# Kernel tuning notes

Hardware: AMD Instinct MI355X
Metric: run time of the kernel (lower is better)

## Reference

```python
import jax, jax.numpy as jnp
import numpy as np
from jax import lax

GAIN = 16.0           # encoder_gains[0]
TEMP = 0.3            # soft_round_temperature
MASK = 9              # mask_size
PAD = 4               # (MASK - 1) // 2
# dim_arm = 16 causal taps inside the 9x9 mask (all indices < center index 40)
CTX_IDX = [12, 13, 14, 20, 21, 22, 23, 24, 28, 29, 30, 31, 32, 33, 38, 39]
CTX_OFF = [(i // MASK, i % MASK) for i in CTX_IDX]
IMG_H, IMG_W = 1024, 1536
N_GRIDS = 7
SIZES = [(int(np.ceil(IMG_H / 2 ** i)), int(np.ceil(IMG_W / 2 ** i))) for i in range(N_GRIDS)]
N_TOTAL = sum(h * w for h, w in SIZES)  # 2097024


def _softround(x, t):
    fl = jnp.floor(x)
    return fl + 0.5 * jnp.tanh((x - fl - 0.5) / t) / jnp.tanh(0.5 / t) + 0.5


def _forward(latents, noise_u, arm_w1, arm_b1, arm_w2, arm_b2, arm_wo, arm_bo,
             ups_k, pre_k, syn_w1, syn_b1, syn_w2, syn_b2):
    # --- quantize latents: softround(softround(x*g) + kumaraswamy noise), a=1 -> uniform-0.5 ---
    flat = jnp.concatenate([l.reshape(-1) for l in latents]) * GAIN
    flat_q = _softround(_softround(flat, TEMP) + (noise_u - 0.5), TEMP)
    dec, cnt = [], 0
    for h, w in SIZES:
        dec.append(flat_q[cnt:cnt + h * w].reshape(1, 1, h, w))
        cnt += h * w
    # --- _get_neighbor: masked causal context gather (16 taps of the 9x9 mask) ---
    ctxs = []
    for l in dec:
        h, w = l.shape[2], l.shape[3]
        xp = jnp.pad(l[0, 0], PAD)  # zero pad, matches F.pad constant 0
        ctxs.append(jnp.stack([xp[dy:dy + h, dx:dx + w] for dy, dx in CTX_OFF], axis=-1).reshape(-1, len(CTX_OFF)))
    ctx = jnp.concatenate(ctxs, axis=0)  # [N, 16]
    # --- ARM MLP: residual hidden layers, final linear to (mu, log_scale) ---
    h1 = jax.nn.relu(ctx @ arm_w1.T + arm_b1 + ctx)
    h2 = jax.nn.relu(h1 @ arm_w2.T + arm_b2 + h1)
    raw = h2 @ arm_wo.T + arm_bo
    mu, log_s = raw[:, 0], raw[:, 1]
    scale = jnp.exp(-0.5 * jnp.clip(log_s, -13.8155, 13.8155))
    def lcdf(x):
        return 0.5 - 0.5 * jnp.sign(x - mu) * jnp.expm1(-jnp.abs(x - mu) / scale)
    proba = jnp.maximum(lcdf(flat_q + 0.5) - lcdf(flat_q - 0.5), 2.0 ** -16)
    rate = -jnp.log2(proba)
    # --- upsampling: coarse-to-fine, depthwise separable convT x2 + preconcat filter ---
    x = dec[-1]
    for step, i in enumerate(range(N_GRIDS - 1, 0, -1)):
        c = x.shape[1]
        kern = jnp.broadcast_to(jnp.outer(ups_k[step], ups_k[step])[None, None], (c, 1, 8, 8))
        x = lax.conv_general_dilated(x, kern, (1, 1), ((4, 4), (4, 4)), lhs_dilation=(2, 2),
                                     dimension_numbers=('NCHW', 'OIHW', 'NCHW'), feature_group_count=c)
        ht, wt = SIZES[i - 1]
        x = x[:, :, :ht, :wt]
        pk2 = jnp.outer(pre_k[step], pre_k[step])[None, None]  # (1,1,7,7)
        t = lax.conv_general_dilated(dec[i - 1], pk2, (1, 1), ((3, 3), (3, 3)),
                                     dimension_numbers=('NCHW', 'OIHW', 'NCHW'))
        x = jnp.concatenate([t, x], axis=1)
    # --- synthesis: 1x1 conv 7->48 relu, 48->6, split mean / log_scale ---
    hid = jax.nn.relu(jnp.einsum('bchw,oc->bohw', x, syn_w1) + syn_b1[None, :, None, None])
    out = jnp.einsum('bchw,oc->bohw', hid, syn_w2) + syn_b2[None, :, None, None]
    pixel_mean, pixel_log_scale = out[:, :3], out[:, 3:]
    # F.interpolate to img_size is identity here (already full resolution)
    decoded = jnp.clip(pixel_mean, 0.0, 1.0)
    return pixel_mean, pixel_log_scale, decoded, rate


def setup_inputs():
    key = jax.random.key(0)
    ks = jax.random.split(key, 16)
    d = {}
    for i, (h, w) in enumerate(SIZES):
        d['latent%d' % i] = jax.random.uniform(ks[i], (1, 1, h, w), jnp.float32, -0.5, 0.5)
    d['noise_u'] = jax.random.uniform(ks[7], (N_TOTAL,), jnp.float32)
    d['arm_w1'] = jax.random.normal(ks[8], (16, 16), jnp.float32) * 0.25
    d['arm_b1'] = jnp.zeros((16,), jnp.float32)
    d['arm_w2'] = jax.random.normal(ks[9], (16, 16), jnp.float32) * 0.25
    d['arm_b2'] = jnp.zeros((16,), jnp.float32)
    d['arm_wo'] = jax.random.normal(ks[10], (2, 16), jnp.float32) * 0.25
    d['arm_bo'] = jnp.zeros((2,), jnp.float32)
    d['ups_k'] = jax.random.normal(ks[11], (6, 8), jnp.float32) * 0.2 + 0.125
    d['pre_k'] = jax.random.normal(ks[12], (6, 7), jnp.float32) * 0.2 + 0.1
    d['syn_w1'] = jax.random.normal(ks[13], (48, 7), jnp.float32) * 0.3
    d['syn_b1'] = jnp.zeros((48,), jnp.float32)
    d['syn_w2'] = jax.random.normal(ks[14], (6, 48), jnp.float32) * 0.1
    d['syn_b2'] = jnp.zeros((6,), jnp.float32)
    return d


def reference(latent0, latent1, latent2, latent3, latent4, latent5, latent6, noise_u,
              arm_w1, arm_b1, arm_w2, arm_b2, arm_wo, arm_bo,
              ups_k, pre_k, syn_w1, syn_b1, syn_w2, syn_b2):
    return _forward([latent0, latent1, latent2, latent3, latent4, latent5, latent6], noise_u,
                    arm_w1, arm_b1, arm_w2, arm_b2, arm_wo, arm_bo,
                    ups_k, pre_k, syn_w1, syn_b1, syn_w2, syn_b2)
```

## Files before the change

kernel.cpp:

```cpp
#include <hip/hip_runtime.h>
#include <math.h>

#define N_TOTAL 2097024
#define HWF (1024 * 1536)

#define OFF0 0
#define OFF1 1572864
#define OFF2 1966080
#define OFF3 2064384
#define OFF4 2088960
#define OFF5 2095104
#define OFF6 2096640

#define OUT_LS   (3 * HWF)
#define OUT_DEC  (6 * HWF)
#define OUT_RATE (9 * HWF)

typedef float f4 __attribute__((ext_vector_type(4), aligned(4)));

__device__ __forceinline__ float softround_f(float x) {
    const float INV_T = 1.0f / 0.3f;
    const float HALF_OVER_TANH = 0.53699381f;
    float fl = floorf(x);
    return fl + tanhf((x - fl - 0.5f) * INV_T) * HALF_OVER_TANH + 0.5f;
}

__global__ void quant_kernel(const float* __restrict__ l0, const float* __restrict__ l1,
                             const float* __restrict__ l2, const float* __restrict__ l3,
                             const float* __restrict__ l4, const float* __restrict__ l5,
                             const float* __restrict__ l6, const float* __restrict__ noise,
                             float* __restrict__ flat_q) {
    int idx = blockIdx.x * blockDim.x + threadIdx.x;
    if (idx >= N_TOTAL) return;
    float v;
    if      (idx < OFF1) v = l0[idx - OFF0];
    else if (idx < OFF2) v = l1[idx - OFF1];
    else if (idx < OFF3) v = l2[idx - OFF2];
    else if (idx < OFF4) v = l3[idx - OFF3];
    else if (idx < OFF5) v = l4[idx - OFF4];
    else if (idx < OFF6) v = l5[idx - OFF5];
    else                 v = l6[idx - OFF6];
    float x = v * 16.0f;
    float s1 = softround_f(x);
    float s2 = softround_f(s1 + noise[idx] - 0.5f);
    flat_q[idx] = s2;
}

template <int H, int W, int OFFT>
__device__ __forceinline__ void arm_body(const float* __restrict__ flat_q, int pos,
                                         const float* __restrict__ w1, const float* __restrict__ b1,
                                         const float* __restrict__ w2, const float* __restrict__ b2,
                                         const float* __restrict__ wo, const float* __restrict__ bo,
                                         float* __restrict__ rate_out) {
    if (pos >= H * W) return;
    unsigned up = (unsigned)pos;
    int y = up / (unsigned)W;
    int x = pos - y * W;
    const float* g = flat_q + OFFT;

    const int DY[16] = {-3,-3,-3,-2,-2,-2,-2,-2,-1,-1,-1,-1,-1,-1, 0, 0};
    const int DX[16] = {-1, 0, 1,-2,-1, 0, 1, 2,-3,-2,-1, 0, 1, 2,-2,-1};
    float ctx[16];
#pragma unroll
    for (int k = 0; k < 16; k++) {
        int yy = y + DY[k], xx = x + DX[k];
        ctx[k] = (yy >= 0 && yy < H && xx >= 0 && xx < W) ? g[yy * W + xx] : 0.0f;
    }

    float h1[16];
#pragma unroll 4
    for (int j = 0; j < 16; j++) {
        float acc = b1[j] + ctx[j];
#pragma unroll
        for (int k = 0; k < 16; k++) acc = fmaf(w1[j * 16 + k], ctx[k], acc);
        h1[j] = fmaxf(acc, 0.0f);
    }
    float h2[16];
#pragma unroll 4
    for (int j = 0; j < 16; j++) {
        float acc = b2[j] + h1[j];
#pragma unroll
        for (int k = 0; k < 16; k++) acc = fmaf(w2[j * 16 + k], h1[k], acc);
        h2[j] = fmaxf(acc, 0.0f);
    }
    float mu = bo[0], ls = bo[1];
#pragma unroll
    for (int k = 0; k < 16; k++) {
        mu = fmaf(wo[k], h2[k], mu);
        ls = fmaf(wo[16 + k], h2[k], ls);
    }
    ls = fminf(fmaxf(ls, -13.8155f), 13.8155f);
    float inv_scale = expf(0.5f * ls);

    float q = g[(size_t)y * W + x];
    float da = (q + 0.5f) - mu;
    float db = (q - 0.5f) - mu;
    float la = 0.5f - 0.5f * copysignf(1.0f, da) * expm1f(-fabsf(da) * inv_scale);
    float lb = 0.5f - 0.5f * copysignf(1.0f, db) * expm1f(-fabsf(db) * inv_scale);
    float proba = fmaxf(la - lb, 1.52587890625e-05f);
    rate_out[OFFT + pos] = -log2f(proba);
}

__global__ __launch_bounds__(256) void arm_all_kernel(
    const float* __restrict__ flat_q,
    const float* __restrict__ w1, const float* __restrict__ b1,
    const float* __restrict__ w2, const float* __restrict__ b2,
    const float* __restrict__ wo, const float* __restrict__ bo,
    float* __restrict__ rate_out) {
    int b = blockIdx.x;
    int t = threadIdx.x;
    if (b < 6144) {
        arm_body<1024, 1536, OFF0>(flat_q, b * 256 + t, w1, b1, w2, b2, wo, bo, rate_out);
    } else if (b < 7680) {
        arm_body<512, 768, OFF1>(flat_q, (b - 6144) * 256 + t, w1, b1, w2, b2, wo, bo, rate_out);
    } else if (b < 8064) {
        arm_body<256, 384, OFF2>(flat_q, (b - 7680) * 256 + t, w1, b1, w2, b2, wo, bo, rate_out);
    } else if (b < 8160) {
        arm_body<128, 192, OFF3>(flat_q, (b - 8064) * 256 + t, w1, b1, w2, b2, wo, bo, rate_out);
    } else if (b < 8184) {
        arm_body<64, 96, OFF4>(flat_q, (b - 8160) * 256 + t, w1, b1, w2, b2, wo, bo, rate_out);
    } else if (b < 8190) {
        arm_body<32, 48, OFF5>(flat_q, (b - 8184) * 256 + t, w1, b1, w2, b2, wo, bo, rate_out);
    } else {
        arm_body<16, 24, OFF6>(flat_q, (b - 8190) * 256 + t, w1, b1, w2, b2, wo, bo, rate_out);
    }
}

__device__ __forceinline__ void up_quad(const float* __restrict__ in, int H, int W,
                                        int i, int j, const float* K, float o[4]) {
    float w[5][5];
    bool interior = (i >= 2 && i <= H - 3 && j >= 2 && j <= W - 3);
    if (interior) {
        const float* p = in + (i - 2) * W + (j - 2);
#pragma unroll
        for (int r = 0; r < 5; r++) {
            f4 a = *(const f4*)p;
            w[r][0] = a.x; w[r][1] = a.y; w[r][2] = a.z; w[r][3] = a.w;
            w[r][4] = p[4];
            p += W;
        }
    } else {
#pragma unroll
        for (int r = 0; r < 5; r++)
#pragma unroll
            for (int e = 0; e < 5; e++) {
                int yy = i - 2 + r, xx = j - 2 + e;
                w[r][e] = (yy >= 0 && yy < H && xx >= 0 && xx < W) ? in[yy * W + xx] : 0.0f;
            }
    }
    float h0[5], h1[5];
#pragma unroll
    for (int r = 0; r < 5; r++) {
        h0[r] = K[0]*w[r][0] + K[2]*w[r][1] + K[4]*w[r][2] + K[6]*w[r][3];
        h1[r] = K[1]*w[r][1] + K[3]*w[r][2] + K[5]*w[r][3] + K[7]*w[r][4];
    }
    o[0] = K[0]*h0[0] + K[2]*h0[1] + K[4]*h0[2] + K[6]*h0[3];
    o[1] = K[0]*h1[0] + K[2]*h1[1] + K[4]*h1[2] + K[6]*h1[3];
    o[2] = K[1]*h0[1] + K[3]*h0[2] + K[5]*h0[3] + K[7]*h0[4];
    o[3] = K[1]*h1[1] + K[3]*h1[2] + K[5]*h1[3] + K[7]*h1[4];
}

__device__ __forceinline__ void conv7_quad(const float* __restrict__ dec, int H, int W,
                                           int i, int j, const float* k, float o[4]) {
    int Y = 2 * i, X = 2 * j;
    float g0[8], g1[8];
    bool interior = (Y - 3 >= 0 && Y + 4 <= H - 1 && X - 3 >= 0 && X + 4 <= W - 1);
    if (interior) {
        const float* p = dec + (Y - 3) * W + (X - 3);
#pragma unroll
        for (int r = 0; r < 8; r++) {
            f4 a = *(const f4*)p;
            f4 b = *(const f4*)(p + 4);
            g0[r] = k[0]*a.x + k[1]*a.y + k[2]*a.z + k[3]*a.w + k[4]*b.x + k[5]*b.y + k[6]*b.z;
            g1[r] = k[0]*a.y + k[1]*a.z + k[2]*a.w + k[3]*b.x + k[4]*b.y + k[5]*b.z + k[6]*b.w;
            p += W;
        }
    } else {
#pragma unroll
        for (int r = 0; r < 8; r++) {
            float wv[8];
#pragma unroll
            for (int q = 0; q < 8; q++) {
                int yy = Y - 3 + r, xx = X - 3 + q;
                wv[q] = (yy >= 0 && yy < H && xx >= 0 && xx < W) ? dec[yy * W + xx] : 0.0f;
            }
            g0[r] = k[0]*wv[0] + k[1]*wv[1] + k[2]*wv[2] + k[3]*wv[3] + k[4]*wv[4] + k[5]*wv[5] + k[6]*wv[6];
            g1[r] = k[0]*wv[1] + k[1]*wv[2] + k[2]*wv[3] + k[3]*wv[4] + k[4]*wv[5] + k[5]*wv[6] + k[6]*wv[7];
        }
    }
    o[0] = k[0]*g0[0] + k[1]*g0[1] + k[2]*g0[2] + k[3]*g0[3] + k[4]*g0[4] + k[5]*g0[5] + k[6]*g0[6];
    o[1] = k[0]*g1[0] + k[1]*g1[1] + k[2]*g1[2] + k[3]*g1[3] + k[4]*g1[4] + k[5]*g1[5] + k[6]*g1[6];
    o[2] = k[0]*g0[1] + k[1]*g0[2] + k[2]*g0[3] + k[3]*g0[4] + k[4]*g0[5] + k[5]*g0[6] + k[6]*g0[7];
    o[3] = k[0]*g1[1] + k[1]*g1[2] + k[2]*g1[3] + k[3]*g1[4] + k[4]*g1[5] + k[5]*g1[6] + k[6]*g1[7];
}

__global__ void pyramid_quad_kernel(const float* __restrict__ xin, int hin, int win_,
                                    const float* __restrict__ dec,
                                    const float* __restrict__ upsk, const float* __restrict__ prek,
                                    float* __restrict__ xout, int hout, int wout) {
    int qw = wout >> 1, qh = hout >> 1;
    int j = blockIdx.x * blockDim.x + threadIdx.x;
    int i = blockIdx.y * blockDim.y + threadIdx.y;
    int c = blockIdx.z;
    if (j >= qw || i >= qh) return;
    float o[4];
    if (c == 0) {
        float k[7];
#pragma unroll
        for (int p = 0; p < 7; p++) k[p] = prek[p];
        conv7_quad(dec, hout, wout, i, j, k, o);
    } else {
        float K[8];
#pragma unroll
        for (int p = 0; p < 8; p++) K[p] = upsk[p];
        up_quad(xin + (size_t)(c - 1) * hin * win_, hin, win_, i, j, K, o);
    }
    size_t base = ((size_t)c * hout + 2 * i) * wout + 2 * j;
    *(float2*)(xout + base)        = make_float2(o[0], o[1]);
    *(float2*)(xout + base + wout) = make_float2(o[2], o[3]);
}

__global__ __launch_bounds__(256) void final_kernel(
    const float* __restrict__ up_in,
    const float* __restrict__ dec0,
    const float* __restrict__ upsk, const float* __restrict__ prek,
    const float* __restrict__ w1, const float* __restrict__ b1,
    const float* __restrict__ w2, const float* __restrict__ b2,
    float* __restrict__ out) {
    const int H2_ = 512, W2_ = 768, H1_ = 1024, W1_ = 1536;
    int t = threadIdx.x;
    int j = blockIdx.x * 16 + (t & 15);
    int i = blockIdx.y * 16 + (t >> 4);

    float K[8], kp[7];
#pragma unroll
    for (int p = 0; p < 8; p++) K[p] = upsk[p];
#pragma unroll
    for (int p = 0; p < 7; p++) kp[p] = prek[p];

    float px0[7], px1[7], px2[7], px3[7];
    {
        float o[4];
        conv7_quad(dec0, H1_, W1_, i, j, kp, o);
        px0[0] = o[0]; px1[0] = o[1]; px2[0] = o[2]; px3[0] = o[3];
    }
#pragma unroll
    for (int c = 0; c < 6; c++) {
        float o[4];
        up_quad(up_in + (size_t)c * (H2_ * W2_), H2_, W2_, i, j, K, o);
        px0[c + 1] = o[0]; px1[c + 1] = o[1]; px2[c + 1] = o[2]; px3[c + 1] = o[3];
    }

    float o0[6], o1[6], o2[6], o3[6];
#pragma unroll
    for (int q = 0; q < 6; q++) {
        float bq = b2[q];
        o0[q] = bq; o1[q] = bq; o2[q] = bq; o3[q] = bq;
    }
#pragma unroll 4
    for (int k = 0; k < 48; k++) {
        float bk = b1[k];
        float a0 = bk, a1 = bk, a2 = bk, a3 = bk;
#pragma unroll
        for (int c = 0; c < 7; c++) {
            float wk = w1[k * 7 + c];
            a0 = fmaf(wk, px0[c], a0);
            a1 = fmaf(wk, px1[c], a1);
            a2 = fmaf(wk, px2[c], a2);
            a3 = fmaf(wk, px3[c], a3);
        }
        a0 = fmaxf(a0, 0.0f); a1 = fmaxf(a1, 0.0f); a2 = fmaxf(a2, 0.0f); a3 = fmaxf(a3, 0.0f);
#pragma unroll
        for (int q = 0; q < 6; q++) {
            float wj = w2[q * 48 + k];
            o0[q] = fmaf(wj, a0, o0[q]);
            o1[q] = fmaf(wj, a1, o1[q]);
            o2[q] = fmaf(wj, a2, o2[q]);
            o3[q] = fmaf(wj, a3, o3[q]);
        }
    }

    size_t base = (size_t)(2 * i) * W1_ + 2 * j;
#pragma unroll
    for (int c = 0; c < 3; c++) {
        *(float2*)(out + (size_t)c * HWF + base)       = make_float2(o0[c], o1[c]);
        *(float2*)(out + (size_t)c * HWF + base + W1_) = make_float2(o2[c], o3[c]);
        *(float2*)(out + OUT_LS + (size_t)c * HWF + base)       = make_float2(o0[c + 3], o1[c + 3]);
        *(float2*)(out + OUT_LS + (size_t)c * HWF + base + W1_) = make_float2(o2[c + 3], o3[c + 3]);
        *(float2*)(out + OUT_DEC + (size_t)c * HWF + base) =
            make_float2(fminf(fmaxf(o0[c], 0.0f), 1.0f), fminf(fmaxf(o1[c], 0.0f), 1.0f));
        *(float2*)(out + OUT_DEC + (size_t)c * HWF + base + W1_) =
            make_float2(fminf(fmaxf(o2[c], 0.0f), 1.0f), fminf(fmaxf(o3[c], 0.0f), 1.0f));
    }
}

extern "C" void kernel_launch(void* const* d_in, const int* in_sizes, int n_in,
                              void* d_out, int out_size, void* d_ws, size_t ws_size,
                              hipStream_t stream) {
    const float* lat[7];
    for (int i = 0; i < 7; i++) lat[i] = (const float*)d_in[i];
    const float* noise  = (const float*)d_in[7];
    const float* arm_w1 = (const float*)d_in[8];
    const float* arm_b1 = (const float*)d_in[9];
    const float* arm_w2 = (const float*)d_in[10];
    const float* arm_b2 = (const float*)d_in[11];
    const float* arm_wo = (const float*)d_in[12];
    const float* arm_bo = (const float*)d_in[13];
    const float* ups_k  = (const float*)d_in[14];
    const float* pre_k  = (const float*)d_in[15];
    const float* syn_w1 = (const float*)d_in[16];
    const float* syn_b1 = (const float*)d_in[17];
    const float* syn_w2 = (const float*)d_in[18];
    const float* syn_b2 = (const float*)d_in[19];
    float* out = (float*)d_out;

    float* flat_q = (float*)d_ws;
    float* bufA   = flat_q + N_TOTAL;
    float* bufB   = bufA + 6 * 512 * 768;

    static const int SH[7]  = {1024, 512, 256, 128, 64, 32, 16};
    static const int SW[7]  = {1536, 768, 384, 192, 96, 48, 24};
    static const int OFF[7] = {OFF0, OFF1, OFF2, OFF3, OFF4, OFF5, OFF6};

    quant_kernel<<<(N_TOTAL + 255) / 256, 256, 0, stream>>>(
        lat[0], lat[1], lat[2], lat[3], lat[4], lat[5], lat[6], noise, flat_q);

    arm_all_kernel<<<8192, 256, 0, stream>>>(flat_q, arm_w1, arm_b1, arm_w2, arm_b2,
                                             arm_wo, arm_bo, out + OUT_RATE);

    const float* xin = flat_q + OFF6;
    float* bufs[2] = {bufA, bufB};
    for (int s = 0; s < 5; s++) {
        int i    = 6 - s;
        int hin  = SH[i], win_ = SW[i];
        int hout = SH[i - 1], wout = SW[i - 1];
        int cin  = s + 1;
        float* xout = bufs[s & 1];
        dim3 blk(16, 16);
        dim3 grd((wout / 2 + 15) / 16, (hout / 2 + 15) / 16, cin + 1);
        pyramid_quad_kernel<<<grd, blk, 0, stream>>>(xin, hin, win_,
                                                     flat_q + OFF[i - 1],
                                                     ups_k + s * 8, pre_k + s * 7,
                                                     xout, hout, wout);
        xin = xout;
    }

    dim3 fgrd(768 / 16, 512 / 16);
    final_kernel<<<fgrd, 256, 0, stream>>>(bufA, flat_q,
                                           ups_k + 5 * 8, pre_k + 5 * 7,
                                           syn_w1, syn_b1, syn_w2, syn_b2, out);
}
```

Before: 149.6 us.

## Use packed FP32 math across ARM, upsampling and synthesis kernels

Rewrites the ARM MLP so each thread handles two adjacent pixels using 2-wide float vectors, which are meant to map to packed FP32 FMA instructions. It adds an interior fast path that loads the context taps as vectors, and halves the ARM grid to match. The upsampling, conv7 and synthesis MLP inner loops are also reorganised around packed FMAs. Softround replaces tanhf with an exp/reciprocal formulation, which may slightly change numerical accuracy; processing two pixels per thread also raises register pressure.

```diff
diff --git a/kernel.cpp b/kernel.cpp
--- a/kernel.cpp
+++ b/kernel.cpp
@@ -16,13 +16,22 @@
 #define OUT_DEC  (6 * HWF)
 #define OUT_RATE (9 * HWF)
 
-typedef float f4 __attribute__((ext_vector_type(4), aligned(4)));
+typedef float f4  __attribute__((ext_vector_type(4), aligned(4)));
+typedef float pf2 __attribute__((ext_vector_type(2), aligned(4)));
+
+__device__ __forceinline__ pf2 splat2(float s) { return (pf2){s, s}; }
+__device__ __forceinline__ pf2 pk_fma(pf2 a, pf2 b, pf2 c) { return __builtin_elementwise_fma(a, b, c); }
+__device__ __forceinline__ pf2 pk_max(pf2 a, pf2 b) { return __builtin_elementwise_max(a, b); }
+__device__ __forceinline__ pf2 pk_min(pf2 a, pf2 b) { return __builtin_elementwise_min(a, b); }
 
 __device__ __forceinline__ float softround_f(float x) {
     const float INV_T = 1.0f / 0.3f;
     const float HALF_OVER_TANH = 0.53699381f;
     float fl = floorf(x);
-    return fl + tanhf((x - fl - 0.5f) * INV_T) * HALF_OVER_TANH + 0.5f;
+    float z = (x - fl - 0.5f) * INV_T;
+    float e = __expf(2.0f * z);
+    float th = 1.0f - 2.0f * __builtin_amdgcn_rcpf(e + 1.0f);
+    return fl + th * HALF_OVER_TANH + 0.5f;
 }
 
 __global__ void quant_kernel(const float* __restrict__ l0, const float* __restrict__ l1,
@@ -47,58 +56,77 @@
 }
 
 template <int H, int W, int OFFT>
-__device__ __forceinline__ void arm_body(const float* __restrict__ flat_q, int pos,
-                                         const float* __restrict__ w1, const float* __restrict__ b1,
-                                         const float* __restrict__ w2, const float* __restrict__ b2,
-                                         const float* __restrict__ wo, const float* __restrict__ bo,
-                                         float* __restrict__ rate_out) {
-    if (pos >= H * W) return;
-    unsigned up = (unsigned)pos;
-    int y = up / (unsigned)W;
+__device__ __forceinline__ void arm_body2(const float* __restrict__ flat_q, int pair,
+                                          const float* __restrict__ w1, const float* __restrict__ b1,
+                                          const float* __restrict__ w2, const float* __restrict__ b2,
+                                          const float* __restrict__ wo, const float* __restrict__ bo,
+                                          float* __restrict__ rate_out) {
+    constexpr int NPAIR = H * W / 2;
+    if (pair >= NPAIR) return;
+    int pos = 2 * pair;
+    int y = (unsigned)pos / (unsigned)W;
     int x = pos - y * W;
     const float* g = flat_q + OFFT;
 
     const int DY[16] = {-3,-3,-3,-2,-2,-2,-2,-2,-1,-1,-1,-1,-1,-1, 0, 0};
     const int DX[16] = {-1, 0, 1,-2,-1, 0, 1, 2,-3,-2,-1, 0, 1, 2,-2,-1};
-    float ctx[16];
-#pragma unroll
-    for (int k = 0; k < 16; k++) {
-        int yy = y + DY[k], xx = x + DX[k];
-        ctx[k] = (yy >= 0 && yy < H && xx >= 0 && xx < W) ? g[yy * W + xx] : 0.0f;
-    }
-
-    float h1[16];
+    pf2 ctx[16];
+    bool interior = (y >= 3) && (x >= 3) && (x <= W - 4);
+    if (interior) {
+#pragma unroll
+        for (int k = 0; k < 16; k++)
+            ctx[k] = *(const pf2*)&g[(y + DY[k]) * W + x + DX[k]];
+    } else {
+#pragma unroll
+        for (int k = 0; k < 16; k++) {
+            int yy = y + DY[k];
+            float lo = 0.0f, hi = 0.0f;
+            if (yy >= 0) {
+                int xx = x + DX[k];
+                if (xx >= 0 && xx < W)          lo = g[yy * W + xx];
+                if (xx + 1 >= 0 && xx + 1 < W)  hi = g[yy * W + xx + 1];
+            }
+            ctx[k] = (pf2){lo, hi};
+        }
+    }
+
+    pf2 h1[16];
 #pragma unroll 4
     for (int j = 0; j < 16; j++) {
-        float acc = b1[j] + ctx[j];
-#pragma unroll
-        for (int k = 0; k < 16; k++) acc = fmaf(w1[j * 16 + k], ctx[k], acc);
-        h1[j] = fmaxf(acc, 0.0f);
-    }
-    float h2[16];
+        pf2 acc = splat2(b1[j]) + ctx[j];
+#pragma unroll
+        for (int k = 0; k < 16; k++) acc = pk_fma(splat2(w1[j * 16 + k]), ctx[k], acc);
+        h1[j] = pk_max(acc, splat2(0.0f));
+    }
+    pf2 h2[16];
 #pragma unroll 4
     for (int j = 0; j < 16; j++) {
-        float acc = b2[j] + h1[j];
-#pragma unroll
-        for (int k = 0; k < 16; k++) acc = fmaf(w2[j * 16 + k], h1[k], acc);
-        h2[j] = fmaxf(acc, 0.0f);
-    }
-    float mu = bo[0], ls = bo[1];
+        pf2 acc = splat2(b2[j]) + h1[j];
+#pragma unroll
+        for (int k = 0; k < 16; k++) acc = pk_fma(splat2(w2[j * 16 + k]), h1[k], acc);
+        h2[j] = pk_max(acc, splat2(0.0f));
+    }
+    pf2 mu = splat2(bo[0]), ls = splat2(bo[1]);
 #pragma unroll
     for (int k = 0; k < 16; k++) {
-        mu = fmaf(wo[k], h2[k], mu);
-        ls = fmaf(wo[16 + k], h2[k], ls);
-    }
-    ls = fminf(fmaxf(ls, -13.8155f), 13.8155f);
-    float inv_scale = expf(0.5f * ls);
-
-    float q = g[(size_t)y * W + x];
-    float da = (q + 0.5f) - mu;
-    float db = (q - 0.5f) - mu;
-    float la = 0.5f - 0.5f * copysignf(1.0f, da) * expm1f(-fabsf(da) * inv_scale);
-    float lb = 0.5f - 0.5f * copysignf(1.0f, db) * expm1f(-fabsf(db) * inv_scale);
-    float proba = fmaxf(la - lb, 1.52587890625e-05f);
-    rate_out[OFFT + pos] = -log2f(proba);
+        mu = pk_fma(splat2(wo[k]), h2[k], mu);
+        ls = pk_fma(splat2(wo[16 + k]), h2[k], ls);
+    }
+
+    pf2 q = *(const pf2*)&g[pos];
+    pf2 rate;
+#pragma unroll
+    for (int c = 0; c < 2; c++) {
+        float lsc = fminf(fmaxf(ls[c], -13.8155f), 13.8155f);
+        float inv_scale = __expf(0.5f * lsc);
+        float da = (q[c] + 0.5f) - mu[c];
+        float db = (q[c] - 0.5f) - mu[c];
+        float la = 0.5f - 0.5f * copysignf(1.0f, da) * expm1f(-fabsf(da) * inv_scale);
+        float lb = 0.5f - 0.5f * copysignf(1.0f, db) * expm1f(-fabsf(db) * inv_scale);
+        float proba = fmaxf(la - lb, 1.52587890625e-05f);
+        rate[c] = -log2f(proba);
+    }
+    *(pf2*)&rate_out[OFFT + pos] = rate;
 }
 
 __global__ __launch_bounds__(256) void arm_all_kernel(
@@ -109,25 +137,25 @@
     float* __restrict__ rate_out) {
     int b = blockIdx.x;
     int t = threadIdx.x;
-    if (b < 6144) {
-        arm_body<1024, 1536, OFF0>(flat_q, b * 256 + t, w1, b1, w2, b2, wo, bo, rate_out);
-    } else if (b < 7680) {
-        arm_body<512, 768, OFF1>(flat_q, (b - 6144) * 256 + t, w1, b1, w2, b2, wo, bo, rate_out);
-    } else if (b < 8064) {
-        arm_body<256, 384, OFF2>(flat_q, (b - 7680) * 256 + t, w1, b1, w2, b2, wo, bo, rate_out);
-    } else if (b < 8160) {
-        arm_body<128, 192, OFF3>(flat_q, (b - 8064) * 256 + t, w1, b1, w2, b2, wo, bo, rate_out);
-    } else if (b < 8184) {
-        arm_body<64, 96, OFF4>(flat_q, (b - 8160) * 256 + t, w1, b1, w2, b2, wo, bo, rate_out);
-    } else if (b < 8190) {
-        arm_body<32, 48, OFF5>(flat_q, (b - 8184) * 256 + t, w1, b1, w2, b2, wo, bo, rate_out);
+    if (b < 3072) {
+        arm_body2<1024, 1536, OFF0>(flat_q, b * 256 + t, w1, b1, w2, b2, wo, bo, rate_out);
+    } else if (b < 3840) {
+        arm_body2<512, 768, OFF1>(flat_q, (b - 3072) * 256 + t, w1, b1, w2, b2, wo, bo, rate_out);
+    } else if (b < 4032) {
+        arm_body2<256, 384, OFF2>(flat_q, (b - 3840) * 256 + t, w1, b1, w2, b2, wo, bo, rate_out);
+    } else if (b < 4080) {
+        arm_body2<128, 192, OFF3>(flat_q, (b - 4032) * 256 + t, w1, b1, w2, b2, wo, bo, rate_out);
+    } else if (b < 4092) {
+        arm_body2<64, 96, OFF4>(flat_q, (b - 4080) * 256 + t, w1, b1, w2, b2, wo, bo, rate_out);
+    } else if (b < 4095) {
+        arm_body2<32, 48, OFF5>(flat_q, (b - 4092) * 256 + t, w1, b1, w2, b2, wo, bo, rate_out);
     } else {
-        arm_body<16, 24, OFF6>(flat_q, (b - 8190) * 256 + t, w1, b1, w2, b2, wo, bo, rate_out);
-    }
-}
-
-__device__ __forceinline__ void up_quad(const float* __restrict__ in, int H, int W,
-                                        int i, int j, const float* K, float o[4]) {
+        arm_body2<16, 24, OFF6>(flat_q, (b - 4095) * 256 + t, w1, b1, w2, b2, wo, bo, rate_out);
+    }
+}
+
+__device__ __forceinline__ void up_quad_pk(const float* __restrict__ in, int H, int W,
+                                           int i, int j, const float* K, pf2& o01, pf2& o23) {
     float w[5][5];
     bool interior = (i >= 2 && i <= H - 3 && j >= 2 && j <= W - 3);
     if (interior) {
@@ -148,50 +176,56 @@
                 w[r][e] = (yy >= 0 && yy < H && xx >= 0 && xx < W) ? in[yy * W + xx] : 0.0f;
             }
     }
-    float h0[5], h1[5];
+    pf2 h01[5];
 #pragma unroll
     for (int r = 0; r < 5; r++) {
-        h0[r] = K[0]*w[r][0] + K[2]*w[r][1] + K[4]*w[r][2] + K[6]*w[r][3];
-        h1[r] = K[1]*w[r][1] + K[3]*w[r][2] + K[5]*w[r][3] + K[7]*w[r][4];
-    }
-    o[0] = K[0]*h0[0] + K[2]*h0[1] + K[4]*h0[2] + K[6]*h0[3];
-    o[1] = K[0]*h1[0] + K[2]*h1[1] + K[4]*h1[2] + K[6]*h1[3];
-    o[2] = K[1]*h0[1] + K[3]*h0[2] + K[5]*h0[3] + K[7]*h0[4];
-    o[3] = K[1]*h1[1] + K[3]*h1[2] + K[5]*h1[3] + K[7]*h1[4];
-}
-
-__device__ __forceinline__ void conv7_quad(const float* __restrict__ dec, int H, int W,
-                                           int i, int j, const float* k, float o[4]) {
+        pf2 acc = splat2(0.0f);
+#pragma unroll
+        for (int e = 0; e < 4; e++)
+            acc = pk_fma((pf2){K[2 * e], K[2 * e + 1]}, (pf2){w[r][e], w[r][e + 1]}, acc);
+        h01[r] = acc;
+    }
+    o01 = splat2(0.0f); o23 = splat2(0.0f);
+#pragma unroll
+    for (int d = 0; d < 4; d++) {
+        o01 = pk_fma(splat2(K[2 * d]),     h01[d],     o01);
+        o23 = pk_fma(splat2(K[2 * d + 1]), h01[d + 1], o23);
+    }
+}
+
+__device__ __forceinline__ void conv7_quad_pk(const float* __restrict__ dec, int H, int W,
+                                              int i, int j, const float* k, pf2& o01, pf2& o23) {
     int Y = 2 * i, X = 2 * j;
-    float g0[8], g1[8];
+    pf2 g01[8];
     bool interior = (Y - 3 >= 0 && Y + 4 <= H - 1 && X - 3 >= 0 && X + 4 <= W - 1);
-    if (interior) {
-        const float* p = dec + (Y - 3) * W + (X - 3);
-#pragma unroll
-        for (int r = 0; r < 8; r++) {
+#pragma unroll
+    for (int r = 0; r < 8; r++) {
+        float wv[8];
+        if (interior) {
+            const float* p = dec + (Y - 3 + r) * W + (X - 3);
             f4 a = *(const f4*)p;
             f4 b = *(const f4*)(p + 4);
-            g0[r] = k[0]*a.x + k[1]*a.y + k[2]*a.z + k[3]*a.w + k[4]*b.x + k[5]*b.y + k[6]*b.z;
-            g1[r] = k[0]*a.y + k[1]*a.z + k[2]*a.w + k[3]*b.x + k[4]*b.y + k[5]*b.z + k[6]*b.w;
-            p += W;
-        }
-    } else {
-#pragma unroll
-        for (int r = 0; r < 8; r++) {
-            float wv[8];
+            wv[0] = a.x; wv[1] = a.y; wv[2] = a.z; wv[3] = a.w;
+            wv[4] = b.x; wv[5] = b.y; wv[6] = b.z; wv[7] = b.w;
+        } else {
 #pragma unroll
             for (int q = 0; q < 8; q++) {
                 int yy = Y - 3 + r, xx = X - 3 + q;
                 wv[q] = (yy >= 0 && yy < H && xx >= 0 && xx < W) ? dec[yy * W + xx] : 0.0f;
             }
-            g0[r] = k[0]*wv[0] + k[1]*wv[1] + k[2]*wv[2] + k[3]*wv[3] + k[4]*wv[4] + k[5]*wv[5] + k[6]*wv[6];
-            g1[r] = k[0]*wv[1] + k[1]*wv[2] + k[2]*wv[3] + k[3]*wv[4] + k[4]*wv[5] + k[5]*wv[6] + k[6]*wv[7];
-        }
-    }
-    o[0] = k[0]*g0[0] + k[1]*g0[1] + k[2]*g0[2] + k[3]*g0[3] + k[4]*g0[4] + k[5]*g0[5] + k[6]*g0[6];
-    o[1] = k[0]*g1[0] + k[1]*g1[1] + k[2]*g1[2] + k[3]*g1[3] + k[4]*g1[4] + k[5]*g1[5] + k[6]*g1[6];
-    o[2] = k[0]*g0[1] + k[1]*g0[2] + k[2]*g0[3] + k[3]*g0[4] + k[4]*g0[5] + k[5]*g0[6] + k[6]*g0[7];
-    o[3] = k[0]*g1[1] + k[1]*g1[2] + k[2]*g1[3] + k[3]*g1[4] + k[4]*g1[5] + k[5]*g1[6] + k[6]*g1[7];
+        }
+        pf2 acc = splat2(0.0f);
+#pragma unroll
+        for (int q = 0; q < 7; q++)
+            acc = pk_fma(splat2(k[q]), (pf2){wv[q], wv[q + 1]}, acc);
+        g01[r] = acc;
+    }
+    o01 = splat2(0.0f); o23 = splat2(0.0f);
+#pragma unroll
+    for (int r = 0; r < 7; r++) {
+        o01 = pk_fma(splat2(k[r]), g01[r],     o01);
+        o23 = pk_fma(splat2(k[r]), g01[r + 1], o23);
+    }
 }
 
 __global__ void pyramid_quad_kernel(const float* __restrict__ xin, int hin, int win_,
@@ -203,21 +237,21 @@
     int i = blockIdx.y * blockDim.y + threadIdx.y;
     int c = blockIdx.z;
     if (j >= qw || i >= qh) return;
-    float o[4];
+    pf2 o01, o23;
     if (c == 0) {
         float k[7];
 #pragma unroll
         for (int p = 0; p < 7; p++) k[p] = prek[p];
-        conv7_quad(dec, hout, wout, i, j, k, o);
+        conv7_quad_pk(dec, hout, wout, i, j, k, o01, o23);
     } else {
         float K[8];
 #pragma unroll
         for (int p = 0; p < 8; p++) K[p] = upsk[p];
-        up_quad(xin + (size_t)(c - 1) * hin * win_, hin, win_, i, j, K, o);
+        up_quad_pk(xin + (size_t)(c - 1) * hin * win_, hin, win_, i, j, K, o01, o23);
     }
     size_t base = ((size_t)c * hout + 2 * i) * wout + 2 * j;
-    *(float2*)(xout + base)        = make_float2(o[0], o[1]);
-    *(float2*)(xout + base + wout) = make_float2(o[2], o[3]);
+    *(pf2*)(xout + base)        = o01;
+    *(pf2*)(xout + base + wout) = o23;
 }
 
 __global__ __launch_bounds__(256) void final_kernel(
@@ -238,59 +272,45 @@
 #pragma unroll
     for (int p = 0; p < 7; p++) kp[p] = prek[p];
 
-    float px0[7], px1[7], px2[7], px3[7];
-    {
-        float o[4];
-        conv7_quad(dec0, H1_, W1_, i, j, kp, o);
-        px0[0] = o[0]; px1[0] = o[1]; px2[0] = o[2]; px3[0] = o[3];
-    }
-#pragma unroll
-    for (int c = 0; c < 6; c++) {
-        float o[4];
-        up_quad(up_in + (size_t)c * (H2_ * W2_), H2_, W2_, i, j, K, o);
-        px0[c + 1] = o[0]; px1[c + 1] = o[1]; px2[c + 1] = o[2]; px3[c + 1] = o[3];
-    }
-
-    float o0[6], o1[6], o2[6], o3[6];
-#pragma unroll
-    for (int q = 0; q < 6; q++) {
-        float bq = b2[q];
-        o0[q] = bq; o1[q] = bq; o2[q] = bq; o3[q] = bq;
-    }
+    pf2 px01[7], px23[7];
+    conv7_quad_pk(dec0, H1_, W1_, i, j, kp, px01[0], px23[0]);
+#pragma unroll
+    for (int c = 0; c < 6; c++)
+        up_quad_pk(up_in + (size_t)c * (H2_ * W2_), H2_, W2_, i, j, K, px01[c + 1], px23[c + 1]);
+
+    pf2 o01[6], o23[6];
+#pragma unroll
+    for (int q = 0; q < 6; q++) { o01[q] = splat2(b2[q]); o23[q] = splat2(b2[q]); }
 #pragma unroll 4
     for (int k = 0; k < 48; k++) {
-        float bk = b1[k];
-        float a0 = bk, a1 = bk, a2 = bk, a3 = bk;
+        pf2 a01 = splat2(b1[k]), a23 = a01;
 #pragma unroll
         for (int c = 0; c < 7; c++) {
-            float wk = w1[k * 7 + c];
-            a0 = fmaf(wk, px0[c], a0);
-            a1 = fmaf(wk, px1[c], a1);
-            a2 = fmaf(wk, px2[c], a2);
-            a3 = fmaf(wk, px3[c], a3);
-        }
-        a0 = fmaxf(a0, 0.0f); a1 = fmaxf(a1, 0.0f); a2 = fmaxf(a2, 0.0f); a3 = fmaxf(a3, 0.0f);
+            pf2 wk = splat2(w1[k * 7 + c]);
+            a01 = pk_fma(wk, px01[c], a01);
+            a23 = pk_fma(wk, px23[c], a23);
+        }
+        a01 = pk_max(a01, splat2(0.0f));
+        a23 = pk_max(a23, splat2(0.0f));
 #pragma unroll
         for (int q = 0; q < 6; q++) {
-            float wj = w2[q * 48 + k];
-            o0[q] = fmaf(wj, a0, o0[q]);
-            o1[q] = fmaf(wj, a1, o1[q]);
-            o2[q] = fmaf(wj, a2, o2[q]);
-            o3[q] = fmaf(wj, a3, o3[q]);
+            pf2 wj = splat2(w2[q * 48 + k]);
+            o01[q] = pk_fma(wj, a01, o01[q]);
+            o23[q] = pk_fma(wj, a23, o23[q]);
         }
     }
 
     size_t base = (size_t)(2 * i) * W1_ + 2 * j;
 #pragma unroll
     for (int c = 0; c < 3; c++) {
-        *(float2*)(out + (size_t)c * HWF + base)       = make_float2(o0[c], o1[c]);
-        *(float2*)(out + (size_t)c * HWF + base + W1_) = make_float2(o2[c], o3[c]);
-        *(float2*)(out + OUT_LS + (size_t)c * HWF + base)       = make_float2(o0[c + 3], o1[c + 3]);
-        *(float2*)(out + OUT_LS + (size_t)c * HWF + base + W1_) = make_float2(o2[c + 3], o3[c + 3]);
-        *(float2*)(out + OUT_DEC + (size_t)c * HWF + base) =
-            make_float2(fminf(fmaxf(o0[c], 0.0f), 1.0f), fminf(fmaxf(o1[c], 0.0f), 1.0f));
-        *(float2*)(out + OUT_DEC + (size_t)c * HWF + base + W1_) =
-            make_float2(fminf(fmaxf(o2[c], 0.0f), 1.0f), fminf(fmaxf(o3[c], 0.0f), 1.0f));
+        *(pf2*)(out + (size_t)c * HWF + base)       = o01[c];
+        *(pf2*)(out + (size_t)c * HWF + base + W1_) = o23[c];
+        *(pf2*)(out + OUT_LS + (size_t)c * HWF + base)       = o01[c + 3];
+        *(pf2*)(out + OUT_LS + (size_t)c * HWF + base + W1_) = o23[c + 3];
+        *(pf2*)(out + OUT_DEC + (size_t)c * HWF + base) =
+            pk_min(pk_max(o01[c], splat2(0.0f)), splat2(1.0f));
+        *(pf2*)(out + OUT_DEC + (size_t)c * HWF + base + W1_) =
+            pk_min(pk_max(o23[c], splat2(0.0f)), splat2(1.0f));
     }
 }
 
@@ -325,7 +345,7 @@
     quant_kernel<<<(N_TOTAL + 255) / 256, 256, 0, stream>>>(
         lat[0], lat[1], lat[2], lat[3], lat[4], lat[5], lat[6], noise, flat_q);
 
-    arm_all_kernel<<<8192, 256, 0, stream>>>(flat_q, arm_w1, arm_b1, arm_w2, arm_b2,
+    arm_all_kernel<<<4096, 256, 0, stream>>>(flat_q, arm_w1, arm_b1, arm_w2, arm_b2,
                                              arm_wo, arm_bo, out + OUT_RATE);
 
     const float* xin = flat_q + OFF6;
```

Result: slower. 174.6 us (+16.8%).

## Merge ARM rate kernel into final synthesis kernel and use fast tanh

Applied to the files above, without the earlier changes.

Removes the standalone ARM kernel and appends its blocks to the final synthesis kernel, so one launch covers both and the heavy final blocks run alongside the ARM blocks. Softround's tanhf is replaced with an exp plus hardware reciprocal formulation to cut transcendental cost in the quantize kernel. The inv_scale line computes a fast exp that is immediately overwritten by the original expf, so that part does nothing. The fused kernel's register use is the larger of the two bodies, which may reduce occupancy for the ARM part, and the fast tanh slightly changes numerics.

```diff
diff --git a/kernel.cpp b/kernel.cpp
--- a/kernel.cpp
+++ b/kernel.cpp
@@ -22,7 +22,10 @@
     const float INV_T = 1.0f / 0.3f;
     const float HALF_OVER_TANH = 0.53699381f;
     float fl = floorf(x);
-    return fl + tanhf((x - fl - 0.5f) * INV_T) * HALF_OVER_TANH + 0.5f;
+    float z = (x - fl - 0.5f) * INV_T;
+    float e = __expf(2.0f * z);
+    float th = 1.0f - 2.0f * __builtin_amdgcn_rcpf(e + 1.0f);
+    return fl + th * HALF_OVER_TANH + 0.5f;
 }
 
 __global__ void quant_kernel(const float* __restrict__ l0, const float* __restrict__ l1,
@@ -90,7 +93,8 @@
         ls = fmaf(wo[16 + k], h2[k], ls);
     }
     ls = fminf(fmaxf(ls, -13.8155f), 13.8155f);
-    float inv_scale = expf(0.5f * ls);
+    float inv_scale = __expf(0.5f * ls * 1.44269504f * 0.69314718f);
+    inv_scale = expf(0.5f * ls);
 
     float q = g[(size_t)y * W + x];
     float da = (q + 0.5f) - mu;
@@ -99,31 +103,6 @@
     float lb = 0.5f - 0.5f * copysignf(1.0f, db) * expm1f(-fabsf(db) * inv_scale);
     float proba = fmaxf(la - lb, 1.52587890625e-05f);
     rate_out[OFFT + pos] = -log2f(proba);
-}
-
-__global__ __launch_bounds__(256) void arm_all_kernel(
-    const float* __restrict__ flat_q,
-    const float* __restrict__ w1, const float* __restrict__ b1,
-    const float* __restrict__ w2, const float* __restrict__ b2,
-    const float* __restrict__ wo, const float* __restrict__ bo,
-    float* __restrict__ rate_out) {
-    int b = blockIdx.x;
-    int t = threadIdx.x;
-    if (b < 6144) {
-        arm_body<1024, 1536, OFF0>(flat_q, b * 256 + t, w1, b1, w2, b2, wo, bo, rate_out);
-    } else if (b < 7680) {
-        arm_body<512, 768, OFF1>(flat_q, (b - 6144) * 256 + t, w1, b1, w2, b2, wo, bo, rate_out);
-    } else if (b < 8064) {
-        arm_body<256, 384, OFF2>(flat_q, (b - 7680) * 256 + t, w1, b1, w2, b2, wo, bo, rate_out);
-    } else if (b < 8160) {
-        arm_body<128, 192, OFF3>(flat_q, (b - 8064) * 256 + t, w1, b1, w2, b2, wo, bo, rate_out);
-    } else if (b < 8184) {
-        arm_body<64, 96, OFF4>(flat_q, (b - 8160) * 256 + t, w1, b1, w2, b2, wo, bo, rate_out);
-    } else if (b < 8190) {
-        arm_body<32, 48, OFF5>(flat_q, (b - 8184) * 256 + t, w1, b1, w2, b2, wo, bo, rate_out);
-    } else {
-        arm_body<16, 24, OFF6>(flat_q, (b - 8190) * 256 + t, w1, b1, w2, b2, wo, bo, rate_out);
-    }
 }
 
 __device__ __forceinline__ void up_quad(const float* __restrict__ in, int H, int W,
@@ -220,7 +199,7 @@
     *(float2*)(xout + base + wout) = make_float2(o[2], o[3]);
 }
 
-__global__ __launch_bounds__(256) void final_kernel(
+__device__ __forceinline__ void final_body(int b, int t,
     const float* __restrict__ up_in,
     const float* __restrict__ dec0,
     const float* __restrict__ upsk, const float* __restrict__ prek,
@@ -228,9 +207,11 @@
     const float* __restrict__ w2, const float* __restrict__ b2,
     float* __restrict__ out) {
     const int H2_ = 512, W2_ = 768, H1_ = 1024, W1_ = 1536;
-    int t = threadIdx.x;
-    int j = blockIdx.x * 16 + (t & 15);
-    int i = blockIdx.y * 16 + (t >> 4);
+    unsigned ub = (unsigned)b;
+    int by = ub / 48u;
+    int bx = b - by * 48;
+    int j = bx * 16 + (t & 15);
+    int i = by * 16 + (t >> 4);
 
     float K[8], kp[7];
 #pragma unroll
@@ -291,6 +272,40 @@
             make_float2(fminf(fmaxf(o0[c], 0.0f), 1.0f), fminf(fmaxf(o1[c], 0.0f), 1.0f));
         *(float2*)(out + OUT_DEC + (size_t)c * HWF + base + W1_) =
             make_float2(fminf(fmaxf(o2[c], 0.0f), 1.0f), fminf(fmaxf(o3[c], 0.0f), 1.0f));
+    }
+}
+
+__global__ __launch_bounds__(256) void mega_kernel(
+    const float* __restrict__ up_in, const float* __restrict__ flat_q,
+    const float* __restrict__ upsk, const float* __restrict__ prek,
+    const float* __restrict__ sw1, const float* __restrict__ sb1,
+    const float* __restrict__ sw2, const float* __restrict__ sb2,
+    const float* __restrict__ aw1, const float* __restrict__ ab1,
+    const float* __restrict__ aw2, const float* __restrict__ ab2,
+    const float* __restrict__ awo, const float* __restrict__ abo,
+    float* __restrict__ out) {
+    int b = blockIdx.x;
+    int t = threadIdx.x;
+    if (b < 1536) {
+        final_body(b, t, up_in, flat_q, upsk, prek, sw1, sb1, sw2, sb2, out);
+        return;
+    }
+    int ab = b - 1536;
+    float* rate_out = out + OUT_RATE;
+    if (ab < 6144) {
+        arm_body<1024, 1536, OFF0>(flat_q, ab * 256 + t, aw1, ab1, aw2, ab2, awo, abo, rate_out);
+    } else if (ab < 7680) {
+        arm_body<512, 768, OFF1>(flat_q, (ab - 6144) * 256 + t, aw1, ab1, aw2, ab2, awo, abo, rate_out);
+    } else if (ab < 8064) {
+        arm_body<256, 384, OFF2>(flat_q, (ab - 7680) * 256 + t, aw1, ab1, aw2, ab2, awo, abo, rate_out);
+    } else if (ab < 8160) {
+        arm_body<128, 192, OFF3>(flat_q, (ab - 8064) * 256 + t, aw1, ab1, aw2, ab2, awo, abo, rate_out);
+    } else if (ab < 8184) {
+        arm_body<64, 96, OFF4>(flat_q, (ab - 8160) * 256 + t, aw1, ab1, aw2, ab2, awo, abo, rate_out);
+    } else if (ab < 8190) {
+        arm_body<32, 48, OFF5>(flat_q, (ab - 8184) * 256 + t, aw1, ab1, aw2, ab2, awo, abo, rate_out);
+    } else {
+        arm_body<16, 24, OFF6>(flat_q, (ab - 8190) * 256 + t, aw1, ab1, aw2, ab2, awo, abo, rate_out);
     }
 }
 
@@ -325,9 +340,6 @@
     quant_kernel<<<(N_TOTAL + 255) / 256, 256, 0, stream>>>(
         lat[0], lat[1], lat[2], lat[3], lat[4], lat[5], lat[6], noise, flat_q);
 
-    arm_all_kernel<<<8192, 256, 0, stream>>>(flat_q, arm_w1, arm_b1, arm_w2, arm_b2,
-                                             arm_wo, arm_bo, out + OUT_RATE);
-
     const float* xin = flat_q + OFF6;
     float* bufs[2] = {bufA, bufB};
     for (int s = 0; s < 5; s++) {
@@ -345,8 +357,9 @@
         xin = xout;
     }
 
-    dim3 fgrd(768 / 16, 512 / 16);
-    final_kernel<<<fgrd, 256, 0, stream>>>(bufA, flat_q,
-                                           ups_k + 5 * 8, pre_k + 5 * 7,
-                                           syn_w1, syn_b1, syn_w2, syn_b2, out);
-}
+    mega_kernel<<<9728, 256, 0, stream>>>(bufA, flat_q,
+                                          ups_k + 5 * 8, pre_k + 5 * 7,
+                                          syn_w1, syn_b1, syn_w2, syn_b2,
+                                          arm_w1, arm_b1, arm_w2, arm_b2,
+                                          arm_wo, arm_bo, out);
+}
```

Result: slower. 169.9 us (+13.6%).

## Run synthesis MLP on fp16 MFMA and use fast exp-based tanh

Applied to the files above, without the earlier changes.

The per-pixel synthesis MLP (7->48->6) in the final kernel now runs as 16x16x16 fp16 MFMA tiles. Pixel features are staged through per-wave shared memory, the bias is folded in as a constant-1 input, and the outputs are written back with a new per-lane store pattern. Softround's tanhf is replaced by an __expf plus hardware reciprocal formulation. This trades FMA-bound scalar math for matrix instructions, but adds fp16 rounding error, less coalesced scalar stores and an approximate tanh.

```diff
diff --git a/kernel.cpp b/kernel.cpp
--- a/kernel.cpp
+++ b/kernel.cpp
@@ -17,12 +17,18 @@
 #define OUT_RATE (9 * HWF)
 
 typedef float f4 __attribute__((ext_vector_type(4), aligned(4)));
+typedef float float4v __attribute__((ext_vector_type(4)));
+typedef _Float16 half4 __attribute__((ext_vector_type(4)));
+typedef _Float16 half8 __attribute__((ext_vector_type(8)));
 
 __device__ __forceinline__ float softround_f(float x) {
     const float INV_T = 1.0f / 0.3f;
     const float HALF_OVER_TANH = 0.53699381f;
     float fl = floorf(x);
-    return fl + tanhf((x - fl - 0.5f) * INV_T) * HALF_OVER_TANH + 0.5f;
+    float z = (x - fl - 0.5f) * INV_T;
+    float e = __expf(2.0f * z);
+    float th = 1.0f - 2.0f * __builtin_amdgcn_rcpf(e + 1.0f);
+    return fl + th * HALF_OVER_TANH + 0.5f;
 }
 
 __global__ void quant_kernel(const float* __restrict__ l0, const float* __restrict__ l1,
@@ -227,10 +233,37 @@
     const float* __restrict__ w1, const float* __restrict__ b1,
     const float* __restrict__ w2, const float* __restrict__ b2,
     float* __restrict__ out) {
+    __shared__ __align__(16) _Float16 stage[4][2048];
+
     const int H2_ = 512, W2_ = 768, H1_ = 1024, W1_ = 1536;
     int t = threadIdx.x;
-    int j = blockIdx.x * 16 + (t & 15);
-    int i = blockIdx.y * 16 + (t >> 4);
+    int lane = t & 63, wv = t >> 6;
+    int lo = lane & 15, lhi = lane >> 4;
+
+    half4 a1f[3], a2f[3];
+#pragma unroll
+    for (int T = 0; T < 3; T++) {
+        int jj = lo + 16 * T;
+#pragma unroll
+        for (int i = 0; i < 4; i++) {
+            int k = 4 * lhi + i;
+            float v1 = 0.0f;
+            if (lhi < 2) v1 = (k < 7) ? w1[jj * 7 + k] : ((k == 7) ? b1[jj] : 0.0f);
+            a1f[T][i] = (_Float16)v1;
+            float v2 = (lo < 6) ? w2[lo * 48 + 16 * T + k] : 0.0f;
+            a2f[T][i] = (_Float16)v2;
+        }
+    }
+    float4v c2init = {0.f, 0.f, 0.f, 0.f};
+#pragma unroll
+    for (int i = 0; i < 4; i++) {
+        int m = 4 * lhi + i;
+        c2init[i] = (m < 6) ? b2[m] : 0.0f;
+    }
+
+    int qx = t & 15, qy = t >> 4;
+    int j = blockIdx.x * 16 + qx;
+    int i = blockIdx.y * 16 + qy;
 
     float K[8], kp[7];
 #pragma unroll
@@ -251,46 +284,80 @@
         px0[c + 1] = o[0]; px1[c + 1] = o[1]; px2[c + 1] = o[2]; px3[c + 1] = o[3];
     }
 
-    float o0[6], o1[6], o2[6], o3[6];
-#pragma unroll
-    for (int q = 0; q < 6; q++) {
-        float bq = b2[q];
-        o0[q] = bq; o1[q] = bq; o2[q] = bq; o3[q] = bq;
-    }
-#pragma unroll 4
-    for (int k = 0; k < 48; k++) {
-        float bk = b1[k];
-        float a0 = bk, a1 = bk, a2 = bk, a3 = bk;
-#pragma unroll
-        for (int c = 0; c < 7; c++) {
-            float wk = w1[k * 7 + c];
-            a0 = fmaf(wk, px0[c], a0);
-            a1 = fmaf(wk, px1[c], a1);
-            a2 = fmaf(wk, px2[c], a2);
-            a3 = fmaf(wk, px3[c], a3);
-        }
-        a0 = fmaxf(a0, 0.0f); a1 = fmaxf(a1, 0.0f); a2 = fmaxf(a2, 0.0f); a3 = fmaxf(a3, 0.0f);
-#pragma unroll
-        for (int q = 0; q < 6; q++) {
-            float wj = w2[q * 48 + k];
-            o0[q] = fmaf(wj, a0, o0[q]);
-            o1[q] = fmaf(wj, a1, o1[q]);
-            o2[q] = fmaf(wj, a2, o2[q]);
-            o3[q] = fmaf(wj, a3, o3[q]);
-        }
-    }
-
-    size_t base = (size_t)(2 * i) * W1_ + 2 * j;
-#pragma unroll
-    for (int c = 0; c < 3; c++) {
-        *(float2*)(out + (size_t)c * HWF + base)       = make_float2(o0[c], o1[c]);
-        *(float2*)(out + (size_t)c * HWF + base + W1_) = make_float2(o2[c], o3[c]);
-        *(float2*)(out + OUT_LS + (size_t)c * HWF + base)       = make_float2(o0[c + 3], o1[c + 3]);
-        *(float2*)(out + OUT_LS + (size_t)c * HWF + base + W1_) = make_float2(o2[c + 3], o3[c + 3]);
-        *(float2*)(out + OUT_DEC + (size_t)c * HWF + base) =
-            make_float2(fminf(fmaxf(o0[c], 0.0f), 1.0f), fminf(fmaxf(o1[c], 0.0f), 1.0f));
-        *(float2*)(out + OUT_DEC + (size_t)c * HWF + base + W1_) =
-            make_float2(fminf(fmaxf(o2[c], 0.0f), 1.0f), fminf(fmaxf(o3[c], 0.0f), 1.0f));
+    _Float16* sbase = stage[wv];
+    int qyl = qy & 3;
+    int r0 = 2 * qyl, x0 = 2 * qx;
+    {
+        const float* pxs[4] = {px0, px1, px2, px3};
+        const int rr[4] = {r0, r0, r0 + 1, r0 + 1};
+        const int xx[4] = {x0, x0 + 1, x0, x0 + 1};
+#pragma unroll
+        for (int q = 0; q < 4; q++) {
+            half8 hv;
+#pragma unroll
+            for (int c = 0; c < 7; c++) hv[c] = (_Float16)pxs[q][c];
+            hv[7] = (_Float16)1.0f;
+            *reinterpret_cast<half8*>(sbase + ((rr[q] * 32 + xx[q]) << 3)) = hv;
+        }
+    }
+
+    int by32 = blockIdx.y * 32, bx32 = blockIdx.x * 32;
+    const float4v zero4 = {0.f, 0.f, 0.f, 0.f};
+
+#pragma unroll
+    for (int chunk = 0; chunk < 4; chunk++) {
+        half4 bf[4];
+#pragma unroll
+        for (int u = 0; u < 4; u++) {
+            int g = chunk * 4 + u;
+            int r = g >> 1, hh = g & 1;
+            bf[u] = (half4){};
+            if (lhi < 2)
+                bf[u] = *reinterpret_cast<const half4*>(
+                    sbase + (((r * 32 + hh * 16 + lo) << 3) + (lhi << 2)));
+        }
+        float4v d1[4][3];
+#pragma unroll
+        for (int u = 0; u < 4; u++)
+#pragma unroll
+            for (int T = 0; T < 3; T++)
+                d1[u][T] = __builtin_amdgcn_mfma_f32_16x16x16f16(a1f[T], bf[u], zero4, 0, 0, 0);
+        half4 hp[4][3];
+#pragma unroll
+        for (int u = 0; u < 4; u++)
+#pragma unroll
+            for (int T = 0; T < 3; T++)
+#pragma unroll
+                for (int q = 0; q < 4; q++)
+                    hp[u][T][q] = (_Float16)fmaxf(d1[u][T][q], 0.0f);
+        float4v acc[4];
+#pragma unroll
+        for (int u = 0; u < 4; u++) {
+            acc[u] = c2init;
+#pragma unroll
+            for (int T = 0; T < 3; T++)
+                acc[u] = __builtin_amdgcn_mfma_f32_16x16x16f16(a2f[T], hp[u][T], acc[u], 0, 0, 0);
+        }
+#pragma unroll
+        for (int u = 0; u < 4; u++) {
+            int g = chunk * 4 + u;
+            int r = g >> 1, hh = g & 1;
+            int Y = by32 + 8 * wv + r;
+            size_t p = (size_t)Y * W1_ + bx32 + 16 * hh + lo;
+            float4v a = acc[u];
+            if (lhi == 0) {
+                out[p]               = a[0];
+                out[HWF + p]         = a[1];
+                out[2 * HWF + p]     = a[2];
+                out[OUT_LS + p]      = a[3];
+                out[OUT_DEC + p]           = fminf(fmaxf(a[0], 0.0f), 1.0f);
+                out[OUT_DEC + HWF + p]     = fminf(fmaxf(a[1], 0.0f), 1.0f);
+                out[OUT_DEC + 2 * HWF + p] = fminf(fmaxf(a[2], 0.0f), 1.0f);
+            } else if (lhi == 1) {
+                out[OUT_LS + HWF + p]     = a[0];
+                out[OUT_LS + 2 * HWF + p] = a[1];
+            }
+        }
     }
 }
 
```

After: 181.0 us. +21.0%, slower.
